# Kernel optimization log

Hardware: AMD Instinct MI355X
Metric: run time of the kernel (lower is better)

Reference implementation:

```python
import jax, jax.numpy as jnp
import numpy as np

DN = ('NCDHW', 'OIDHW', 'NCDHW')  # torch Conv3d layout

def conv3d(x, w, b, pad):
    y = jax.lax.conv_general_dilated(x, w, (1, 1, 1), [(p, p) for p in pad], dimension_numbers=DN)
    return y + b[None, :, None, None, None]

def setup_inputs() -> dict:
    key = jax.random.key(0)
    ks = jax.random.split(key, 10)
    C, Cq = 64, 8  # in_channels, in_channels // 8
    s = 0.05
    x = jax.random.normal(ks[0], (2, C, 16, 16, 16), dtype=jnp.float32)
    return {
        'x': x,
        'wq': jax.random.normal(ks[1], (Cq, C, 1, 3, 1), jnp.float32) * s,
        'bq': jax.random.normal(ks[2], (Cq,), jnp.float32) * s,
        'wk': jax.random.normal(ks[3], (Cq, C, 3, 1, 1), jnp.float32) * s,
        'bk': jax.random.normal(ks[4], (Cq,), jnp.float32) * s,
        'wj': jax.random.normal(ks[5], (Cq, C, 1, 1, 3), jnp.float32) * s,
        'bj': jax.random.normal(ks[6], (Cq,), jnp.float32) * s,
        'wv': jax.random.normal(ks[7], (C, C, 1, 1, 1), jnp.float32) * s,
        'bv': jax.random.normal(ks[8], (C,), jnp.float32) * s,
        'gamma': jax.random.normal(ks[9], (1,), jnp.float32) * s,
    }

def reference(x, wq, bq, wk, bk, wj, bj, wv, bv, gamma):
    B, C, H, W, D = x.shape
    N = H * W * D
    q = conv3d(x, wq, bq, (0, 1, 0)).reshape(B, -1, N)   # [B, c, N]
    k = conv3d(x, wk, bk, (1, 0, 0)).reshape(B, -1, N)   # [B, c, N]
    j = conv3d(x, wj, bj, (0, 0, 1)).reshape(B, -1, N)   # [B, c, N]
    # affinity = (Q^T K) (J^T K) reassociated as Q^T (K J^T) K  -- identical math,
    # O(N^2 c) instead of O(N^3) since c = C//8 << N.
    kj = jnp.einsum('bcn,bdn->bcd', k, j)                # [B, c, c] = K @ J^T
    aff = jnp.einsum('bcn,bcd,bdm->bnm', q, kj, k)       # [B, N, N]
    aff = jax.nn.softmax(aff, axis=-1)
    v = conv3d(x, wv, bv, (0, 0, 0)).reshape(B, C, N)    # [B, C, N]
    weights = jnp.einsum('bcn,bnm->bcm', v, aff).reshape(B, C, H, W, D)
    return gamma * weights + x
```

## Files before the change

kernel.cpp:

```cpp
#include <hip/hip_runtime.h>

#define N 4096
#define CIN 64
#define NB 2

typedef unsigned short u16;
typedef short bf16x8 __attribute__((ext_vector_type(8)));
typedef float f32x4 __attribute__((ext_vector_type(4)));

#define OFF_QT 0
#define OFF_KT (OFF_QT + NB*N*8)
#define OFF_JT (OFF_KT + NB*N*8)
#define OFF_V  (OFF_JT + NB*N*8)
#define OFF_QK (OFF_V + NB*CIN*N)
#define OFF_MX (OFF_QK + NB*N*8)
#define OFF_SC (OFF_MX + NB*N)

__device__ __forceinline__ u16 f2bf(float f) {
    union { float f; unsigned u; } v; v.f = f;
    unsigned r = (v.u + 0x7fffu + ((v.u >> 16) & 1u)) >> 16;
    return (u16)r;
}

__global__ __launch_bounds__(256) void prep(
        const float* __restrict__ x,
        const float* __restrict__ wq, const float* __restrict__ bq,
        const float* __restrict__ wk, const float* __restrict__ bk,
        const float* __restrict__ wj, const float* __restrict__ bj,
        const float* __restrict__ wv, const float* __restrict__ bv,
        float* __restrict__ ws, u16* __restrict__ vbf, float* __restrict__ out) {
    int n = blockIdx.x * 256 + threadIdx.x;
    int y = blockIdx.y;
    int b = blockIdx.z;
    const float* xb = x + (size_t)b * CIN * N + n;

    if (y < 8) {
        int cq = y;
        int d = n & 15, w = (n >> 4) & 15, h = n >> 8;
        int owl = (w > 0) ? -16 : 0,  owh = (w < 15) ? 16 : 0;
        int ohl = (h > 0) ? -256 : 0, ohh = (h < 15) ? 256 : 0;
        int odl = (d > 0) ? -1 : 0,   odh = (d < 15) ? 1 : 0;
        float mwl = (w > 0) ? 1.f : 0.f, mwh = (w < 15) ? 1.f : 0.f;
        float mhl = (h > 0) ? 1.f : 0.f, mhh = (h < 15) ? 1.f : 0.f;
        float mdl = (d > 0) ? 1.f : 0.f, mdh = (d < 15) ? 1.f : 0.f;
        float q = bq[cq], k = bk[cq], j = bj[cq];
        for (int c0 = 0; c0 < CIN; c0 += 8) {
            float xc[8], xwl[8], xwh[8], xhl[8], xhh[8], xdl[8], xdh[8];
#pragma unroll
            for (int u = 0; u < 8; ++u) {
                const float* p = xb + (size_t)(c0 + u) * N;
                xc[u]  = p[0];
                xwl[u] = p[owl]; xwh[u] = p[owh];
                xhl[u] = p[ohl]; xhh[u] = p[ohh];
                xdl[u] = p[odl]; xdh[u] = p[odh];
            }
#pragma unroll
            for (int u = 0; u < 8; ++u) {
                int c = c0 + u;
                const float* wqr = wq + (cq * CIN + c) * 3;
                const float* wkr = wk + (cq * CIN + c) * 3;
                const float* wjr = wj + (cq * CIN + c) * 3;
                q += wqr[0] * (xwl[u] * mwl) + wqr[1] * xc[u] + wqr[2] * (xwh[u] * mwh);
                k += wkr[0] * (xhl[u] * mhl) + wkr[1] * xc[u] + wkr[2] * (xhh[u] * mhh);
                j += wjr[0] * (xdl[u] * mdl) + wjr[1] * xc[u] + wjr[2] * (xdh[u] * mdh);
            }
        }
        size_t base = (size_t)(b * N + n) * 8 + cq;
        ws[OFF_QT + base] = q;
        ws[OFF_KT + base] = k;
        ws[OFF_JT + base] = j;
    } else {
        int yy = y - 8;
        int co0 = yy * 8;
        float acc[8];
#pragma unroll
        for (int i = 0; i < 8; ++i) acc[i] = bv[co0 + i];
        for (int c0 = 0; c0 < CIN; c0 += 8) {
            float xv[8];
#pragma unroll
            for (int u = 0; u < 8; ++u) xv[u] = xb[(size_t)(c0 + u) * N];
#pragma unroll
            for (int u = 0; u < 8; ++u)
#pragma unroll
                for (int i = 0; i < 8; ++i)
                    acc[i] += wv[(co0 + i) * CIN + c0 + u] * xv[u];
            if ((c0 >> 3) == yy) {
#pragma unroll
                for (int u = 0; u < 8; ++u)
                    out[(size_t)(b * CIN + c0 + u) * N + n] = xv[u];
            }
        }
#pragma unroll
        for (int i = 0; i < 8; ++i)
            vbf[(size_t)(b * CIN + co0 + i) * N + n] = f2bf(acc[i]);
    }
}

__global__ __launch_bounds__(256) void kjqkj(const float* __restrict__ ws_in,
                                             float* __restrict__ ws) {
    __shared__ float kjpart[4][64];
    __shared__ float kjs[64];
    const int t = threadIdx.x, lane = t & 63, wid = t >> 6;
    const int b = blockIdx.y;
    const float* ktb = ws_in + OFF_KT + (size_t)b * N * 8;
    const float* jtb = ws_in + OFF_JT + (size_t)b * N * 8;
    const float* qtb = ws_in + OFF_QT + (size_t)b * N * 8;

    float acc[64];
#pragma unroll
    for (int i = 0; i < 64; ++i) acc[i] = 0.f;
    for (int i = 0; i < 16; ++i) {
        int nn = i * 256 + t;
        const float4* kt = (const float4*)(ktb + (size_t)nn * 8);
        const float4* jt = (const float4*)(jtb + (size_t)nn * 8);
        float4 ka = kt[0], kb = kt[1], ja = jt[0], jb = jt[1];
        float kv[8] = {ka.x, ka.y, ka.z, ka.w, kb.x, kb.y, kb.z, kb.w};
        float jv[8] = {ja.x, ja.y, ja.z, ja.w, jb.x, jb.y, jb.z, jb.w};
#pragma unroll
        for (int c = 0; c < 8; ++c)
#pragma unroll
            for (int dd = 0; dd < 8; ++dd) acc[c * 8 + dd] += kv[c] * jv[dd];
    }
#pragma unroll
    for (int s = 32; s >= 1; s >>= 1)
#pragma unroll
        for (int i = 0; i < 64; ++i) acc[i] += __shfl_down(acc[i], s, 64);
    if (lane == 0) {
#pragma unroll
        for (int i = 0; i < 64; ++i) kjpart[wid][i] = acc[i];
    }
    __syncthreads();
    if (t < 64) kjs[t] = kjpart[0][t] + kjpart[1][t] + kjpart[2][t] + kjpart[3][t];
    __syncthreads();

    float kjr[64];
#pragma unroll
    for (int i = 0; i < 64; ++i) kjr[i] = kjs[i];
    int m = blockIdx.x * 256 + t;
    const float4* qt = (const float4*)(qtb + (size_t)m * 8);
    float4 qa = qt[0], qb = qt[1];
    float qv[8] = {qa.x, qa.y, qa.z, qa.w, qb.x, qb.y, qb.z, qb.w};
    float o[8];
#pragma unroll
    for (int dd = 0; dd < 8; ++dd) {
        float a = 0.f;
#pragma unroll
        for (int c = 0; c < 8; ++c) a += qv[c] * kjr[c * 8 + dd];
        o[dd] = a;
    }
    float4* dst = (float4*)(ws + OFF_QK + (size_t)(b * N + m) * 8);
    dst[0] = make_float4(o[0], o[1], o[2], o[3]);
    dst[1] = make_float4(o[4], o[5], o[6], o[7]);
}

__global__ __launch_bounds__(256) void pass1(const float* __restrict__ ws,
                                             float* __restrict__ mx_o, float* __restrict__ sc_o,
                                             const float* __restrict__ gamma) {
    int wid = threadIdx.x >> 6, lane = threadIdx.x & 63;
    int gw = blockIdx.x * 4 + wid;
    int r0 = gw * 4;
    int b = r0 >> 12;
    float4 qa[4], qb[4];
#pragma unroll
    for (int rr = 0; rr < 4; ++rr) {
        const float4* q4 = (const float4*)(ws + OFF_QK + (size_t)(r0 + rr) * 8);
        qa[rr] = q4[0]; qb[rr] = q4[1];
    }
    const float* ktb = ws + OFF_KT + (size_t)b * N * 8;
    float mx[4], sm[4];
#pragma unroll
    for (int rr = 0; rr < 4; ++rr) { mx[rr] = -3.0e38f; sm[rr] = 0.f; }
#pragma unroll 4
    for (int i = 0; i < 64; ++i) {
        int m = i * 64 + lane;
        const float4* kk4 = (const float4*)(ktb + (size_t)m * 8);
        float4 ka = kk4[0], kb = kk4[1];
#pragma unroll
        for (int rr = 0; rr < 4; ++rr) {
            float a = qa[rr].x * ka.x + qa[rr].y * ka.y + qa[rr].z * ka.z + qa[rr].w * ka.w
                    + qb[rr].x * kb.x + qb[rr].y * kb.y + qb[rr].z * kb.z + qb[rr].w * kb.w;
            float nm = fmaxf(mx[rr], a);
            sm[rr] = sm[rr] * __expf(mx[rr] - nm) + __expf(a - nm);
            mx[rr] = nm;
        }
    }
#pragma unroll
    for (int s = 32; s >= 1; s >>= 1)
#pragma unroll
        for (int rr = 0; rr < 4; ++rr) {
            float omx = __shfl_xor(mx[rr], s, 64);
            float osm = __shfl_xor(sm[rr], s, 64);
            float nm = fmaxf(mx[rr], omx);
            sm[rr] = sm[rr] * __expf(mx[rr] - nm) + osm * __expf(omx - nm);
            mx[rr] = nm;
        }
    if (lane == 0) {
        float g = gamma[0];
#pragma unroll
        for (int rr = 0; rr < 4; ++rr) {
            mx_o[r0 + rr] = mx[rr];
            sc_o[r0 + rr] = g / sm[rr];
        }
    }
}

__global__ __launch_bounds__(256) void pass2(const float* __restrict__ ws,
                                             const u16* __restrict__ vbf,
                                             float* __restrict__ out) {
    __shared__ u16 Pt[64][72];
    __shared__ u16 Vt[64][72];
    __shared__ float ks[64][8];
    const int t  = threadIdx.x;
    const int b  = blockIdx.z;
    const int m0 = blockIdx.x * 64;
    const int ns = blockIdx.y;
    const float* qkT = ws + OFF_QK + (size_t)b * N * 8;
    const float* ktb = ws + OFF_KT + (size_t)b * N * 8;
    const float* mxv = ws + OFF_MX + (size_t)b * N;
    const float* scv = ws + OFF_SC + (size_t)b * N;
    const u16*   vb  = vbf + (size_t)b * CIN * N;

    if (t < 128) ((float4*)ks)[t] = ((const float4*)(ktb + (size_t)m0 * 8))[t];

    const int lane = t & 63;
    const int wid  = t >> 6;
    const int l16  = lane & 15;
    const int lq   = lane >> 4;
    const int vc   = t >> 3;
    const int vseg = t & 7;

    f32x4 acc[4];
#pragma unroll
    for (int i = 0; i < 4; ++i) acc[i] = (f32x4){0.f, 0.f, 0.f, 0.f};

    for (int ch = 0; ch < 8; ++ch) {
        const int n0 = ns * 512 + ch * 64;
        const int n  = n0 + lane;
        const float4* q4 = (const float4*)(qkT + (size_t)n * 8);
        float4 qa = q4[0], qb = q4[1];
        float mxl = mxv[n], sl = scv[n];
        uint4 v0 = *(const uint4*)(vb + (size_t)vc        * N + n0 + vseg * 8);
        uint4 v1 = *(const uint4*)(vb + (size_t)(vc + 32) * N + n0 + vseg * 8);
        __syncthreads();
#pragma unroll
        for (int r = 0; r < 16; ++r) {
            int mi = wid * 16 + r;
            float4 k0 = *(const float4*)&ks[mi][0];
            float4 k1 = *(const float4*)&ks[mi][4];
            float a = qa.x * k0.x + qa.y * k0.y + qa.z * k0.z + qa.w * k0.w
                    + qb.x * k1.x + qb.y * k1.y + qb.z * k1.z + qb.w * k1.w;
            Pt[mi][lane] = f2bf(__expf(a - mxl) * sl);
        }
        *(uint4*)&Vt[vc][vseg * 8]      = v0;
        *(uint4*)&Vt[vc + 32][vseg * 8] = v1;
        __syncthreads();
#pragma unroll
        for (int kk = 0; kk < 2; ++kk) {
            int k0i = kk * 32 + lq * 8;
            bf16x8 bfrag = *(const bf16x8*)&Pt[wid * 16 + l16][k0i];
#pragma unroll
            for (int ct = 0; ct < 4; ++ct) {
                bf16x8 afrag = *(const bf16x8*)&Vt[ct * 16 + l16][k0i];
                acc[ct] = __builtin_amdgcn_mfma_f32_16x16x32_bf16(afrag, bfrag, acc[ct], 0, 0, 0);
            }
        }
    }
    float* ob = out + (size_t)b * CIN * N;
    const int mcol = m0 + wid * 16 + l16;
#pragma unroll
    for (int ct = 0; ct < 4; ++ct)
#pragma unroll
        for (int r = 0; r < 4; ++r) {
            int c = ct * 16 + lq * 4 + r;
            atomicAdd(&ob[(size_t)c * N + mcol], acc[ct][r]);
        }
}

extern "C" void kernel_launch(void* const* d_in, const int* in_sizes, int n_in,
                              void* d_out, int out_size, void* d_ws, size_t ws_size,
                              hipStream_t stream) {
    const float* x  = (const float*)d_in[0];
    const float* wq = (const float*)d_in[1];
    const float* bq = (const float*)d_in[2];
    const float* wk = (const float*)d_in[3];
    const float* bk = (const float*)d_in[4];
    const float* wj = (const float*)d_in[5];
    const float* bj = (const float*)d_in[6];
    const float* wv = (const float*)d_in[7];
    const float* bv = (const float*)d_in[8];
    const float* gamma = (const float*)d_in[9];
    float* ws  = (float*)d_ws;
    float* out = (float*)d_out;
    u16* vbf = (u16*)(ws + OFF_V);

    prep<<<dim3(16, 16, 2), 256, 0, stream>>>(x, wq, bq, wk, bk, wj, bj, wv, bv, ws, vbf, out);
    kjqkj<<<dim3(16, 2), 256, 0, stream>>>(ws, ws);
    pass1<<<512, 256, 0, stream>>>(ws, ws + OFF_MX, ws + OFF_SC, gamma);
    pass2<<<dim3(64, 8, 2), 256, 0, stream>>>(ws, vbf, out);
}
```

Before: 155.9 us.

## Fuse four kernels into one persistent kernel with grid barriers

Merges prep, kjqkj, pass1 and pass2 into a single 512-block kernel that uses atomic-counter grid barriers between phases, so three kernel launches and their gaps are gone. Each block now recomputes the KJ reduction redundantly and computes QK for its own rows inline before the softmax statistics. Pass2 moves from 1024 blocks over 512-column chunks to 512 blocks over 1024-column chunks, which halves the atomic adds but lowers parallelism. The design depends on all 512 blocks being resident at once (launch_bounds 256,2) and adds a memset to reset the barrier counters.

New measurement: 243.5 us. 56.2% more time.

```diff
diff --git a/kernel.cpp b/kernel.cpp
--- a/kernel.cpp
+++ b/kernel.cpp
@@ -3,6 +3,7 @@
 #define N 4096
 #define CIN 64
 #define NB 2
+#define NBLK 512u
 
 typedef unsigned short u16;
 typedef short bf16x8 __attribute__((ext_vector_type(8)));
@@ -15,6 +16,7 @@
 #define OFF_QK (OFF_V + NB*CIN*N)
 #define OFF_MX (OFF_QK + NB*N*8)
 #define OFF_SC (OFF_MX + NB*N)
+#define OFF_BAR (OFF_SC + NB*N)
 
 __device__ __forceinline__ u16 f2bf(float f) {
     union { float f; unsigned u; } v; v.f = f;
@@ -22,258 +24,275 @@
     return (u16)r;
 }
 
-__global__ __launch_bounds__(256) void prep(
+__device__ __forceinline__ void grid_barrier(unsigned* bar) {
+    __syncthreads();
+    if (threadIdx.x == 0) {
+        __hip_atomic_fetch_add(bar, 1u, __ATOMIC_RELEASE, __HIP_MEMORY_SCOPE_AGENT);
+        while (__hip_atomic_load(bar, __ATOMIC_RELAXED, __HIP_MEMORY_SCOPE_AGENT) < NBLK)
+            __builtin_amdgcn_s_sleep(2);
+        __threadfence();
+    }
+    __syncthreads();
+}
+
+struct SmemB { float kjpart[4][64]; float kjs[64]; };
+struct SmemC { u16 Pt[64][72]; u16 Vt[64][72]; float ks[64][8]; };
+union Smem { SmemB b; SmemC c; };
+
+__global__ __launch_bounds__(256, 2) void fused(
         const float* __restrict__ x,
         const float* __restrict__ wq, const float* __restrict__ bq,
         const float* __restrict__ wk, const float* __restrict__ bk,
         const float* __restrict__ wj, const float* __restrict__ bj,
         const float* __restrict__ wv, const float* __restrict__ bv,
+        const float* __restrict__ gamma,
         float* __restrict__ ws, u16* __restrict__ vbf, float* __restrict__ out) {
-    int n = blockIdx.x * 256 + threadIdx.x;
-    int y = blockIdx.y;
-    int b = blockIdx.z;
-    const float* xb = x + (size_t)b * CIN * N + n;
-
-    if (y < 8) {
-        int cq = y;
-        int d = n & 15, w = (n >> 4) & 15, h = n >> 8;
-        int owl = (w > 0) ? -16 : 0,  owh = (w < 15) ? 16 : 0;
-        int ohl = (h > 0) ? -256 : 0, ohh = (h < 15) ? 256 : 0;
-        int odl = (d > 0) ? -1 : 0,   odh = (d < 15) ? 1 : 0;
-        float mwl = (w > 0) ? 1.f : 0.f, mwh = (w < 15) ? 1.f : 0.f;
-        float mhl = (h > 0) ? 1.f : 0.f, mhh = (h < 15) ? 1.f : 0.f;
-        float mdl = (d > 0) ? 1.f : 0.f, mdh = (d < 15) ? 1.f : 0.f;
-        float q = bq[cq], k = bk[cq], j = bj[cq];
-        for (int c0 = 0; c0 < CIN; c0 += 8) {
-            float xc[8], xwl[8], xwh[8], xhl[8], xhh[8], xdl[8], xdh[8];
-#pragma unroll
-            for (int u = 0; u < 8; ++u) {
-                const float* p = xb + (size_t)(c0 + u) * N;
-                xc[u]  = p[0];
-                xwl[u] = p[owl]; xwh[u] = p[owh];
-                xhl[u] = p[ohl]; xhh[u] = p[ohh];
-                xdl[u] = p[odl]; xdh[u] = p[odh];
-            }
-#pragma unroll
-            for (int u = 0; u < 8; ++u) {
-                int c = c0 + u;
-                const float* wqr = wq + (cq * CIN + c) * 3;
-                const float* wkr = wk + (cq * CIN + c) * 3;
-                const float* wjr = wj + (cq * CIN + c) * 3;
-                q += wqr[0] * (xwl[u] * mwl) + wqr[1] * xc[u] + wqr[2] * (xwh[u] * mwh);
-                k += wkr[0] * (xhl[u] * mhl) + wkr[1] * xc[u] + wkr[2] * (xhh[u] * mhh);
-                j += wjr[0] * (xdl[u] * mdl) + wjr[1] * xc[u] + wjr[2] * (xdh[u] * mdh);
-            }
-        }
-        size_t base = (size_t)(b * N + n) * 8 + cq;
-        ws[OFF_QT + base] = q;
-        ws[OFF_KT + base] = k;
-        ws[OFF_JT + base] = j;
-    } else {
-        int yy = y - 8;
-        int co0 = yy * 8;
-        float acc[8];
-#pragma unroll
-        for (int i = 0; i < 8; ++i) acc[i] = bv[co0 + i];
-        for (int c0 = 0; c0 < CIN; c0 += 8) {
-            float xv[8];
-#pragma unroll
-            for (int u = 0; u < 8; ++u) xv[u] = xb[(size_t)(c0 + u) * N];
-#pragma unroll
-            for (int u = 0; u < 8; ++u)
-#pragma unroll
-                for (int i = 0; i < 8; ++i)
-                    acc[i] += wv[(co0 + i) * CIN + c0 + u] * xv[u];
-            if ((c0 >> 3) == yy) {
+    __shared__ __align__(16) Smem shm;
+    const int t   = threadIdx.x;
+    const int blk = blockIdx.x;
+    unsigned* bar = (unsigned*)(ws + OFF_BAR);
+
+    {
+        const int bx = blk & 15;
+        const int y  = (blk >> 4) & 15;
+        const int b  = blk >> 8;
+        const int n  = bx * 256 + t;
+        const float* xb = x + (size_t)b * CIN * N + n;
+
+        if (y < 8) {
+            int cq = y;
+            int d = n & 15, w = (n >> 4) & 15, h = n >> 8;
+            int owl = (w > 0) ? -16 : 0,  owh = (w < 15) ? 16 : 0;
+            int ohl = (h > 0) ? -256 : 0, ohh = (h < 15) ? 256 : 0;
+            int odl = (d > 0) ? -1 : 0,   odh = (d < 15) ? 1 : 0;
+            float mwl = (w > 0) ? 1.f : 0.f, mwh = (w < 15) ? 1.f : 0.f;
+            float mhl = (h > 0) ? 1.f : 0.f, mhh = (h < 15) ? 1.f : 0.f;
+            float mdl = (d > 0) ? 1.f : 0.f, mdh = (d < 15) ? 1.f : 0.f;
+            float q = bq[cq], k = bk[cq], j = bj[cq];
+            for (int c0 = 0; c0 < CIN; c0 += 8) {
+                float xc[8], xwl[8], xwh[8], xhl[8], xhh[8], xdl[8], xdh[8];
+#pragma unroll
+                for (int u = 0; u < 8; ++u) {
+                    const float* p = xb + (size_t)(c0 + u) * N;
+                    xc[u]  = p[0];
+                    xwl[u] = p[owl]; xwh[u] = p[owh];
+                    xhl[u] = p[ohl]; xhh[u] = p[ohh];
+                    xdl[u] = p[odl]; xdh[u] = p[odh];
+                }
+#pragma unroll
+                for (int u = 0; u < 8; ++u) {
+                    int c = c0 + u;
+                    const float* wqr = wq + (cq * CIN + c) * 3;
+                    const float* wkr = wk + (cq * CIN + c) * 3;
+                    const float* wjr = wj + (cq * CIN + c) * 3;
+                    q += wqr[0] * (xwl[u] * mwl) + wqr[1] * xc[u] + wqr[2] * (xwh[u] * mwh);
+                    k += wkr[0] * (xhl[u] * mhl) + wkr[1] * xc[u] + wkr[2] * (xhh[u] * mhh);
+                    j += wjr[0] * (xdl[u] * mdl) + wjr[1] * xc[u] + wjr[2] * (xdh[u] * mdh);
+                }
+            }
+            size_t base = (size_t)(b * N + n) * 8 + cq;
+            ws[OFF_QT + base] = q;
+            ws[OFF_KT + base] = k;
+            ws[OFF_JT + base] = j;
+        } else {
+            int yy = y - 8;
+            int co0 = yy * 8;
+            float acc[8];
+#pragma unroll
+            for (int i = 0; i < 8; ++i) acc[i] = bv[co0 + i];
+            for (int c0 = 0; c0 < CIN; c0 += 8) {
+                float xv[8];
+#pragma unroll
+                for (int u = 0; u < 8; ++u) xv[u] = xb[(size_t)(c0 + u) * N];
 #pragma unroll
                 for (int u = 0; u < 8; ++u)
-                    out[(size_t)(b * CIN + c0 + u) * N + n] = xv[u];
-            }
-        }
-#pragma unroll
-        for (int i = 0; i < 8; ++i)
-            vbf[(size_t)(b * CIN + co0 + i) * N + n] = f2bf(acc[i]);
+#pragma unroll
+                    for (int i = 0; i < 8; ++i)
+                        acc[i] += wv[(co0 + i) * CIN + c0 + u] * xv[u];
+                if ((c0 >> 3) == yy) {
+#pragma unroll
+                    for (int u = 0; u < 8; ++u)
+                        out[(size_t)(b * CIN + c0 + u) * N + n] = xv[u];
+                }
+            }
+#pragma unroll
+            for (int i = 0; i < 8; ++i)
+                vbf[(size_t)(b * CIN + co0 + i) * N + n] = f2bf(acc[i]);
+        }
     }
-}
-
-__global__ __launch_bounds__(256) void kjqkj(const float* __restrict__ ws_in,
-                                             float* __restrict__ ws) {
-    __shared__ float kjpart[4][64];
-    __shared__ float kjs[64];
-    const int t = threadIdx.x, lane = t & 63, wid = t >> 6;
-    const int b = blockIdx.y;
-    const float* ktb = ws_in + OFF_KT + (size_t)b * N * 8;
-    const float* jtb = ws_in + OFF_JT + (size_t)b * N * 8;
-    const float* qtb = ws_in + OFF_QT + (size_t)b * N * 8;
-
-    float acc[64];
-#pragma unroll
-    for (int i = 0; i < 64; ++i) acc[i] = 0.f;
-    for (int i = 0; i < 16; ++i) {
-        int nn = i * 256 + t;
-        const float4* kt = (const float4*)(ktb + (size_t)nn * 8);
-        const float4* jt = (const float4*)(jtb + (size_t)nn * 8);
-        float4 ka = kt[0], kb = kt[1], ja = jt[0], jb = jt[1];
-        float kv[8] = {ka.x, ka.y, ka.z, ka.w, kb.x, kb.y, kb.z, kb.w};
-        float jv[8] = {ja.x, ja.y, ja.z, ja.w, jb.x, jb.y, jb.z, jb.w};
-#pragma unroll
-        for (int c = 0; c < 8; ++c)
-#pragma unroll
-            for (int dd = 0; dd < 8; ++dd) acc[c * 8 + dd] += kv[c] * jv[dd];
+
+    grid_barrier(bar + 0);
+
+    {
+        const int lane = t & 63, wid = t >> 6;
+        const int b    = blk >> 8;
+        const float* ktb = ws + OFF_KT + (size_t)b * N * 8;
+        const float* jtb = ws + OFF_JT + (size_t)b * N * 8;
+
+        float acc[64];
+#pragma unroll
+        for (int i = 0; i < 64; ++i) acc[i] = 0.f;
+        for (int i = 0; i < 16; ++i) {
+            int nn = i * 256 + t;
+            const float4* kt = (const float4*)(ktb + (size_t)nn * 8);
+            const float4* jt = (const float4*)(jtb + (size_t)nn * 8);
+            float4 ka = kt[0], kb2 = kt[1], ja = jt[0], jb2 = jt[1];
+            float kv[8] = {ka.x, ka.y, ka.z, ka.w, kb2.x, kb2.y, kb2.z, kb2.w};
+            float jv[8] = {ja.x, ja.y, ja.z, ja.w, jb2.x, jb2.y, jb2.z, jb2.w};
+#pragma unroll
+            for (int c = 0; c < 8; ++c)
+#pragma unroll
+                for (int dd = 0; dd < 8; ++dd) acc[c * 8 + dd] += kv[c] * jv[dd];
+        }
+#pragma unroll
+        for (int s = 32; s >= 1; s >>= 1)
+#pragma unroll
+            for (int i = 0; i < 64; ++i) acc[i] += __shfl_down(acc[i], s, 64);
+        if (lane == 0) {
+#pragma unroll
+            for (int i = 0; i < 64; ++i) shm.b.kjpart[wid][i] = acc[i];
+        }
+        __syncthreads();
+        if (t < 64)
+            shm.b.kjs[t] = shm.b.kjpart[0][t] + shm.b.kjpart[1][t]
+                         + shm.b.kjpart[2][t] + shm.b.kjpart[3][t];
+        __syncthreads();
+
+        float kjr[64];
+#pragma unroll
+        for (int i = 0; i < 64; ++i) kjr[i] = shm.b.kjs[i];
+        const int r0 = blk * 16 + wid * 4;
+        float4 qa[4], qb[4];
+#pragma unroll
+        for (int rr = 0; rr < 4; ++rr) {
+            const float4* q4 = (const float4*)(ws + OFF_QT + (size_t)(r0 + rr) * 8);
+            float4 a4 = q4[0], b4 = q4[1];
+            float qv[8] = {a4.x, a4.y, a4.z, a4.w, b4.x, b4.y, b4.z, b4.w};
+            float o[8];
+#pragma unroll
+            for (int dd = 0; dd < 8; ++dd) {
+                float a = 0.f;
+#pragma unroll
+                for (int c = 0; c < 8; ++c) a += qv[c] * kjr[c * 8 + dd];
+                o[dd] = a;
+            }
+            qa[rr] = make_float4(o[0], o[1], o[2], o[3]);
+            qb[rr] = make_float4(o[4], o[5], o[6], o[7]);
+        }
+        if (lane < 32) {
+            const int rr = lane >> 3, dd = lane & 7;
+            const float* qr = ws + OFF_QT + (size_t)(r0 + rr) * 8;
+            float o = 0.f;
+#pragma unroll
+            for (int c = 0; c < 8; ++c) o += qr[c] * shm.b.kjs[c * 8 + dd];
+            ws[OFF_QK + (size_t)r0 * 8 + lane] = o;
+        }
+
+        float mx[4], sm2[4];
+#pragma unroll
+        for (int rr = 0; rr < 4; ++rr) { mx[rr] = -3.0e38f; sm2[rr] = 0.f; }
+#pragma unroll 4
+        for (int i = 0; i < 64; ++i) {
+            const int m = i * 64 + lane;
+            const float4* kk4 = (const float4*)(ktb + (size_t)m * 8);
+            float4 ka = kk4[0], kb2 = kk4[1];
+#pragma unroll
+            for (int rr = 0; rr < 4; ++rr) {
+                float a = qa[rr].x * ka.x + qa[rr].y * ka.y + qa[rr].z * ka.z + qa[rr].w * ka.w
+                        + qb[rr].x * kb2.x + qb[rr].y * kb2.y + qb[rr].z * kb2.z + qb[rr].w * kb2.w;
+                float nm = fmaxf(mx[rr], a);
+                sm2[rr] = sm2[rr] * __expf(mx[rr] - nm) + __expf(a - nm);
+                mx[rr] = nm;
+            }
+        }
+#pragma unroll
+        for (int s = 32; s >= 1; s >>= 1)
+#pragma unroll
+            for (int rr = 0; rr < 4; ++rr) {
+                float omx = __shfl_xor(mx[rr], s, 64);
+                float osm = __shfl_xor(sm2[rr], s, 64);
+                float nm = fmaxf(mx[rr], omx);
+                sm2[rr] = sm2[rr] * __expf(mx[rr] - nm) + osm * __expf(omx - nm);
+                mx[rr] = nm;
+            }
+        if (lane == 0) {
+            float g = gamma[0];
+#pragma unroll
+            for (int rr = 0; rr < 4; ++rr) {
+                ws[OFF_MX + r0 + rr] = mx[rr];
+                ws[OFF_SC + r0 + rr] = g / sm2[rr];
+            }
+        }
     }
-#pragma unroll
-    for (int s = 32; s >= 1; s >>= 1)
-#pragma unroll
-        for (int i = 0; i < 64; ++i) acc[i] += __shfl_down(acc[i], s, 64);
-    if (lane == 0) {
-#pragma unroll
-        for (int i = 0; i < 64; ++i) kjpart[wid][i] = acc[i];
+
+    grid_barrier(bar + 1);
+
+    {
+        const int mt = blk & 63;
+        const int ns = (blk >> 6) & 3;
+        const int b  = blk >> 8;
+        const int m0 = mt * 64;
+        const float* qkT = ws + OFF_QK + (size_t)b * N * 8;
+        const float* ktb = ws + OFF_KT + (size_t)b * N * 8;
+        const float* mxv = ws + OFF_MX + (size_t)b * N;
+        const float* scv = ws + OFF_SC + (size_t)b * N;
+        const u16*   vb  = vbf + (size_t)b * CIN * N;
+
+        if (t < 128) ((float4*)shm.c.ks)[t] = ((const float4*)(ktb + (size_t)m0 * 8))[t];
+
+        const int lane = t & 63;
+        const int wid  = t >> 6;
+        const int l16  = lane & 15;
+        const int lq   = lane >> 4;
+        const int vc   = t >> 3;
+        const int vseg = t & 7;
+
+        f32x4 acc[4];
+#pragma unroll
+        for (int i = 0; i < 4; ++i) acc[i] = (f32x4){0.f, 0.f, 0.f, 0.f};
+
+        for (int ch = 0; ch < 16; ++ch) {
+            const int n0 = ns * 1024 + ch * 64;
+            const int n  = n0 + lane;
+            const float4* q4 = (const float4*)(qkT + (size_t)n * 8);
+            float4 qa = q4[0], qb = q4[1];
+            float mxl = mxv[n], sl = scv[n];
+            uint4 v0 = *(const uint4*)(vb + (size_t)vc        * N + n0 + vseg * 8);
+            uint4 v1 = *(const uint4*)(vb + (size_t)(vc + 32) * N + n0 + vseg * 8);
+            __syncthreads();
+#pragma unroll
+            for (int r = 0; r < 16; ++r) {
+                int mi = wid * 16 + r;
+                float4 k0 = *(const float4*)&shm.c.ks[mi][0];
+                float4 k1 = *(const float4*)&shm.c.ks[mi][4];
+                float a = qa.x * k0.x + qa.y * k0.y + qa.z * k0.z + qa.w * k0.w
+                        + qb.x * k1.x + qb.y * k1.y + qb.z * k1.z + qb.w * k1.w;
+                shm.c.Pt[mi][lane] = f2bf(__expf(a - mxl) * sl);
+            }
+            *(uint4*)&shm.c.Vt[vc][vseg * 8]      = v0;
+            *(uint4*)&shm.c.Vt[vc + 32][vseg * 8] = v1;
+            __syncthreads();
+#pragma unroll
+            for (int kk = 0; kk < 2; ++kk) {
+                int k0i = kk * 32 + lq * 8;
+                bf16x8 bfrag = *(const bf16x8*)&shm.c.Pt[wid * 16 + l16][k0i];
+#pragma unroll
+                for (int ct = 0; ct < 4; ++ct) {
+                    bf16x8 afrag = *(const bf16x8*)&shm.c.Vt[ct * 16 + l16][k0i];
+                    acc[ct] = __builtin_amdgcn_mfma_f32_16x16x32_bf16(afrag, bfrag, acc[ct], 0, 0, 0);
+                }
+            }
+        }
+        float* ob = out + (size_t)b * CIN * N;
+        const int mcol = m0 + wid * 16 + l16;
+#pragma unroll
+        for (int ct = 0; ct < 4; ++ct)
+#pragma unroll
+            for (int r = 0; r < 4; ++r) {
+                int c = ct * 16 + lq * 4 + r;
+                atomicAdd(&ob[(size_t)c * N + mcol], acc[ct][r]);
+            }
     }
-    __syncthreads();
-    if (t < 64) kjs[t] = kjpart[0][t] + kjpart[1][t] + kjpart[2][t] + kjpart[3][t];
-    __syncthreads();
-
-    float kjr[64];
-#pragma unroll
-    for (int i = 0; i < 64; ++i) kjr[i] = kjs[i];
-    int m = blockIdx.x * 256 + t;
-    const float4* qt = (const float4*)(qtb + (size_t)m * 8);
-    float4 qa = qt[0], qb = qt[1];
-    float qv[8] = {qa.x, qa.y, qa.z, qa.w, qb.x, qb.y, qb.z, qb.w};
-    float o[8];
-#pragma unroll
-    for (int dd = 0; dd < 8; ++dd) {
-        float a = 0.f;
-#pragma unroll
-        for (int c = 0; c < 8; ++c) a += qv[c] * kjr[c * 8 + dd];
-        o[dd] = a;
-    }
-    float4* dst = (float4*)(ws + OFF_QK + (size_t)(b * N + m) * 8);
-    dst[0] = make_float4(o[0], o[1], o[2], o[3]);
-    dst[1] = make_float4(o[4], o[5], o[6], o[7]);
-}
-
-__global__ __launch_bounds__(256) void pass1(const float* __restrict__ ws,
-                                             float* __restrict__ mx_o, float* __restrict__ sc_o,
-                                             const float* __restrict__ gamma) {
-    int wid = threadIdx.x >> 6, lane = threadIdx.x & 63;
-    int gw = blockIdx.x * 4 + wid;
-    int r0 = gw * 4;
-    int b = r0 >> 12;
-    float4 qa[4], qb[4];
-#pragma unroll
-    for (int rr = 0; rr < 4; ++rr) {
-        const float4* q4 = (const float4*)(ws + OFF_QK + (size_t)(r0 + rr) * 8);
-        qa[rr] = q4[0]; qb[rr] = q4[1];
-    }
-    const float* ktb = ws + OFF_KT + (size_t)b * N * 8;
-    float mx[4], sm[4];
-#pragma unroll
-    for (int rr = 0; rr < 4; ++rr) { mx[rr] = -3.0e38f; sm[rr] = 0.f; }
-#pragma unroll 4
-    for (int i = 0; i < 64; ++i) {
-        int m = i * 64 + lane;
-        const float4* kk4 = (const float4*)(ktb + (size_t)m * 8);
-        float4 ka = kk4[0], kb = kk4[1];
-#pragma unroll
-        for (int rr = 0; rr < 4; ++rr) {
-            float a = qa[rr].x * ka.x + qa[rr].y * ka.y + qa[rr].z * ka.z + qa[rr].w * ka.w
-                    + qb[rr].x * kb.x + qb[rr].y * kb.y + qb[rr].z * kb.z + qb[rr].w * kb.w;
-            float nm = fmaxf(mx[rr], a);
-            sm[rr] = sm[rr] * __expf(mx[rr] - nm) + __expf(a - nm);
-            mx[rr] = nm;
-        }
-    }
-#pragma unroll
-    for (int s = 32; s >= 1; s >>= 1)
-#pragma unroll
-        for (int rr = 0; rr < 4; ++rr) {
-            float omx = __shfl_xor(mx[rr], s, 64);
-            float osm = __shfl_xor(sm[rr], s, 64);
-            float nm = fmaxf(mx[rr], omx);
-            sm[rr] = sm[rr] * __expf(mx[rr] - nm) + osm * __expf(omx - nm);
-            mx[rr] = nm;
-        }
-    if (lane == 0) {
-        float g = gamma[0];
-#pragma unroll
-        for (int rr = 0; rr < 4; ++rr) {
-            mx_o[r0 + rr] = mx[rr];
-            sc_o[r0 + rr] = g / sm[rr];
-        }
-    }
-}
-
-__global__ __launch_bounds__(256) void pass2(const float* __restrict__ ws,
-                                             const u16* __restrict__ vbf,
-                                             float* __restrict__ out) {
-    __shared__ u16 Pt[64][72];
-    __shared__ u16 Vt[64][72];
-    __shared__ float ks[64][8];
-    const int t  = threadIdx.x;
-    const int b  = blockIdx.z;
-    const int m0 = blockIdx.x * 64;
-    const int ns = blockIdx.y;
-    const float* qkT = ws + OFF_QK + (size_t)b * N * 8;
-    const float* ktb = ws + OFF_KT + (size_t)b * N * 8;
-    const float* mxv = ws + OFF_MX + (size_t)b * N;
-    const float* scv = ws + OFF_SC + (size_t)b * N;
-    const u16*   vb  = vbf + (size_t)b * CIN * N;
-
-    if (t < 128) ((float4*)ks)[t] = ((const float4*)(ktb + (size_t)m0 * 8))[t];
-
-    const int lane = t & 63;
-    const int wid  = t >> 6;
-    const int l16  = lane & 15;
-    const int lq   = lane >> 4;
-    const int vc   = t >> 3;
-    const int vseg = t & 7;
-
-    f32x4 acc[4];
-#pragma unroll
-    for (int i = 0; i < 4; ++i) acc[i] = (f32x4){0.f, 0.f, 0.f, 0.f};
-
-    for (int ch = 0; ch < 8; ++ch) {
-        const int n0 = ns * 512 + ch * 64;
-        const int n  = n0 + lane;
-        const float4* q4 = (const float4*)(qkT + (size_t)n * 8);
-        float4 qa = q4[0], qb = q4[1];
-        float mxl = mxv[n], sl = scv[n];
-        uint4 v0 = *(const uint4*)(vb + (size_t)vc        * N + n0 + vseg * 8);
-        uint4 v1 = *(const uint4*)(vb + (size_t)(vc + 32) * N + n0 + vseg * 8);
-        __syncthreads();
-#pragma unroll
-        for (int r = 0; r < 16; ++r) {
-            int mi = wid * 16 + r;
-            float4 k0 = *(const float4*)&ks[mi][0];
-            float4 k1 = *(const float4*)&ks[mi][4];
-            float a = qa.x * k0.x + qa.y * k0.y + qa.z * k0.z + qa.w * k0.w
-                    + qb.x * k1.x + qb.y * k1.y + qb.z * k1.z + qb.w * k1.w;
-            Pt[mi][lane] = f2bf(__expf(a - mxl) * sl);
-        }
-        *(uint4*)&Vt[vc][vseg * 8]      = v0;
-        *(uint4*)&Vt[vc + 32][vseg * 8] = v1;
-        __syncthreads();
-#pragma unroll
-        for (int kk = 0; kk < 2; ++kk) {
-            int k0i = kk * 32 + lq * 8;
-            bf16x8 bfrag = *(const bf16x8*)&Pt[wid * 16 + l16][k0i];
-#pragma unroll
-            for (int ct = 0; ct < 4; ++ct) {
-                bf16x8 afrag = *(const bf16x8*)&Vt[ct * 16 + l16][k0i];
-                acc[ct] = __builtin_amdgcn_mfma_f32_16x16x32_bf16(afrag, bfrag, acc[ct], 0, 0, 0);
-            }
-        }
-    }
-    float* ob = out + (size_t)b * CIN * N;
-    const int mcol = m0 + wid * 16 + l16;
-#pragma unroll
-    for (int ct = 0; ct < 4; ++ct)
-#pragma unroll
-        for (int r = 0; r < 4; ++r) {
-            int c = ct * 16 + lq * 4 + r;
-            atomicAdd(&ob[(size_t)c * N + mcol], acc[ct][r]);
-        }
 }
 
 extern "C" void kernel_launch(void* const* d_in, const int* in_sizes, int n_in,
@@ -293,8 +312,7 @@
     float* out = (float*)d_out;
     u16* vbf = (u16*)(ws + OFF_V);
 
-    prep<<<dim3(16, 16, 2), 256, 0, stream>>>(x, wq, bq, wk, bk, wj, bj, wv, bv, ws, vbf, out);
-    kjqkj<<<dim3(16, 2), 256, 0, stream>>>(ws, ws);
-    pass1<<<512, 256, 0, stream>>>(ws, ws + OFF_MX, ws + OFF_SC, gamma);
-    pass2<<<dim3(64, 8, 2), 256, 0, stream>>>(ws, vbf, out);
+    hipMemsetAsync(ws + OFF_BAR, 0, 2 * sizeof(unsigned), stream);
+    fused<<<dim3(512), dim3(256), 0, stream>>>(x, wq, bq, wk, bk, wj, bj, wv, bv,
+                                               gamma, ws, vbf, out);
 }
```

## Fuse KJ/QK computation into softmax stats kernel and split channel reduction in prep

Applied to the files above, without the earlier changes.

Merges the kjqkj and pass1 kernels into one statsB kernel. Each block recomputes the 8x8 K·J^T product redundantly, derives its own QK rows, and splits the key range across two half-blocks whose partial max/sum are merged in shared memory. The prep kernel also moves to 512 threads, with each half summing 32 input channels and the halves combined through shared memory. The goal is to drop one launch and improve parallelism, at the cost of recomputing the KJ reduction over all N in each of the 512 blocks.

After: 178.2 us. +14.3%, slower.

```diff
diff --git a/kernel.cpp b/kernel.cpp
--- a/kernel.cpp
+++ b/kernel.cpp
@@ -22,17 +22,25 @@
     return (u16)r;
 }
 
-__global__ __launch_bounds__(256) void prep(
+__global__ __launch_bounds__(512, 4) void prep(
         const float* __restrict__ x,
         const float* __restrict__ wq, const float* __restrict__ bq,
         const float* __restrict__ wk, const float* __restrict__ bk,
         const float* __restrict__ wj, const float* __restrict__ bj,
         const float* __restrict__ wv, const float* __restrict__ bv,
         float* __restrict__ ws, u16* __restrict__ vbf, float* __restrict__ out) {
-    int n = blockIdx.x * 256 + threadIdx.x;
-    int y = blockIdx.y;
-    int b = blockIdx.z;
+    __shared__ union {
+        float qkj[3][256];
+        float accv[256][8];
+    } sh;
+    const int t    = threadIdx.x;
+    const int tn   = t & 255;
+    const int half = t >> 8;
+    const int y    = blockIdx.y;
+    const int b    = blockIdx.z;
+    const int n    = blockIdx.x * 256 + tn;
     const float* xb = x + (size_t)b * CIN * N + n;
+    const int c0base = half * 32;
 
     if (y < 8) {
         int cq = y;
@@ -43,8 +51,11 @@
         float mwl = (w > 0) ? 1.f : 0.f, mwh = (w < 15) ? 1.f : 0.f;
         float mhl = (h > 0) ? 1.f : 0.f, mhh = (h < 15) ? 1.f : 0.f;
         float mdl = (d > 0) ? 1.f : 0.f, mdh = (d < 15) ? 1.f : 0.f;
-        float q = bq[cq], k = bk[cq], j = bj[cq];
-        for (int c0 = 0; c0 < CIN; c0 += 8) {
+        float q = half ? 0.f : bq[cq];
+        float k = half ? 0.f : bk[cq];
+        float j = half ? 0.f : bj[cq];
+        for (int c0i = 0; c0i < 32; c0i += 8) {
+            const int c0 = c0base + c0i;
             float xc[8], xwl[8], xwh[8], xhl[8], xhh[8], xdl[8], xdh[8];
 #pragma unroll
             for (int u = 0; u < 8; ++u) {
@@ -65,17 +76,23 @@
                 j += wjr[0] * (xdl[u] * mdl) + wjr[1] * xc[u] + wjr[2] * (xdh[u] * mdh);
             }
         }
-        size_t base = (size_t)(b * N + n) * 8 + cq;
-        ws[OFF_QT + base] = q;
-        ws[OFF_KT + base] = k;
-        ws[OFF_JT + base] = j;
+        if (half) { sh.qkj[0][tn] = q; sh.qkj[1][tn] = k; sh.qkj[2][tn] = j; }
+        __syncthreads();
+        if (!half) {
+            q += sh.qkj[0][tn]; k += sh.qkj[1][tn]; j += sh.qkj[2][tn];
+            size_t base = (size_t)(b * N + n) * 8 + cq;
+            ws[OFF_QT + base] = q;
+            ws[OFF_KT + base] = k;
+            ws[OFF_JT + base] = j;
+        }
     } else {
         int yy = y - 8;
         int co0 = yy * 8;
         float acc[8];
 #pragma unroll
-        for (int i = 0; i < 8; ++i) acc[i] = bv[co0 + i];
-        for (int c0 = 0; c0 < CIN; c0 += 8) {
+        for (int i = 0; i < 8; ++i) acc[i] = half ? 0.f : bv[co0 + i];
+        for (int c0i = 0; c0i < 32; c0i += 8) {
+            const int c0 = c0base + c0i;
             float xv[8];
 #pragma unroll
             for (int u = 0; u < 8; ++u) xv[u] = xb[(size_t)(c0 + u) * N];
@@ -90,32 +107,40 @@
                     out[(size_t)(b * CIN + c0 + u) * N + n] = xv[u];
             }
         }
-#pragma unroll
-        for (int i = 0; i < 8; ++i)
-            vbf[(size_t)(b * CIN + co0 + i) * N + n] = f2bf(acc[i]);
-    }
-}
-
-__global__ __launch_bounds__(256) void kjqkj(const float* __restrict__ ws_in,
-                                             float* __restrict__ ws) {
-    __shared__ float kjpart[4][64];
+        if (half) {
+#pragma unroll
+            for (int i = 0; i < 8; ++i) sh.accv[tn][i] = acc[i];
+        }
+        __syncthreads();
+        if (!half) {
+#pragma unroll
+            for (int i = 0; i < 8; ++i)
+                vbf[(size_t)(b * CIN + co0 + i) * N + n] = f2bf(acc[i] + sh.accv[tn][i]);
+        }
+    }
+}
+
+__global__ __launch_bounds__(512, 4) void statsB(float* __restrict__ ws,
+                                                 const float* __restrict__ gamma) {
+    __shared__ float kjpart[8][64];
     __shared__ float kjs[64];
+    __shared__ float mxs[8][4], sms[8][4];
     const int t = threadIdx.x, lane = t & 63, wid = t >> 6;
-    const int b = blockIdx.y;
-    const float* ktb = ws_in + OFF_KT + (size_t)b * N * 8;
-    const float* jtb = ws_in + OFF_JT + (size_t)b * N * 8;
-    const float* qtb = ws_in + OFF_QT + (size_t)b * N * 8;
+    const int blk = blockIdx.x;
+    const int b   = blk >> 8;
+    const float* ktb = ws + OFF_KT + (size_t)b * N * 8;
+    const float* jtb = ws + OFF_JT + (size_t)b * N * 8;
 
     float acc[64];
 #pragma unroll
     for (int i = 0; i < 64; ++i) acc[i] = 0.f;
-    for (int i = 0; i < 16; ++i) {
-        int nn = i * 256 + t;
+    for (int i = 0; i < 8; ++i) {
+        int nn = i * 512 + t;
         const float4* kt = (const float4*)(ktb + (size_t)nn * 8);
         const float4* jt = (const float4*)(jtb + (size_t)nn * 8);
-        float4 ka = kt[0], kb = kt[1], ja = jt[0], jb = jt[1];
-        float kv[8] = {ka.x, ka.y, ka.z, ka.w, kb.x, kb.y, kb.z, kb.w};
-        float jv[8] = {ja.x, ja.y, ja.z, ja.w, jb.x, jb.y, jb.z, jb.w};
+        float4 ka = kt[0], kb2 = kt[1], ja = jt[0], jb2 = jt[1];
+        float kv[8] = {ka.x, ka.y, ka.z, ka.w, kb2.x, kb2.y, kb2.z, kb2.w};
+        float jv[8] = {ja.x, ja.y, ja.z, ja.w, jb2.x, jb2.y, jb2.z, jb2.w};
 #pragma unroll
         for (int c = 0; c < 8; ++c)
 #pragma unroll
@@ -130,57 +155,57 @@
         for (int i = 0; i < 64; ++i) kjpart[wid][i] = acc[i];
     }
     __syncthreads();
-    if (t < 64) kjs[t] = kjpart[0][t] + kjpart[1][t] + kjpart[2][t] + kjpart[3][t];
+    if (t < 64)
+        kjs[t] = kjpart[0][t] + kjpart[1][t] + kjpart[2][t] + kjpart[3][t]
+               + kjpart[4][t] + kjpart[5][t] + kjpart[6][t] + kjpart[7][t];
     __syncthreads();
 
     float kjr[64];
 #pragma unroll
     for (int i = 0; i < 64; ++i) kjr[i] = kjs[i];
-    int m = blockIdx.x * 256 + t;
-    const float4* qt = (const float4*)(qtb + (size_t)m * 8);
-    float4 qa = qt[0], qb = qt[1];
-    float qv[8] = {qa.x, qa.y, qa.z, qa.w, qb.x, qb.y, qb.z, qb.w};
-    float o[8];
-#pragma unroll
-    for (int dd = 0; dd < 8; ++dd) {
-        float a = 0.f;
-#pragma unroll
-        for (int c = 0; c < 8; ++c) a += qv[c] * kjr[c * 8 + dd];
-        o[dd] = a;
-    }
-    float4* dst = (float4*)(ws + OFF_QK + (size_t)(b * N + m) * 8);
-    dst[0] = make_float4(o[0], o[1], o[2], o[3]);
-    dst[1] = make_float4(o[4], o[5], o[6], o[7]);
-}
-
-__global__ __launch_bounds__(256) void pass1(const float* __restrict__ ws,
-                                             float* __restrict__ mx_o, float* __restrict__ sc_o,
-                                             const float* __restrict__ gamma) {
-    int wid = threadIdx.x >> 6, lane = threadIdx.x & 63;
-    int gw = blockIdx.x * 4 + wid;
-    int r0 = gw * 4;
-    int b = r0 >> 12;
+    const int wrow  = wid & 3;
+    const int mhalf = wid >> 2;
+    const int r0 = blk * 16 + wrow * 4;
     float4 qa[4], qb[4];
 #pragma unroll
     for (int rr = 0; rr < 4; ++rr) {
-        const float4* q4 = (const float4*)(ws + OFF_QK + (size_t)(r0 + rr) * 8);
-        qa[rr] = q4[0]; qb[rr] = q4[1];
-    }
-    const float* ktb = ws + OFF_KT + (size_t)b * N * 8;
-    float mx[4], sm[4];
-#pragma unroll
-    for (int rr = 0; rr < 4; ++rr) { mx[rr] = -3.0e38f; sm[rr] = 0.f; }
+        const float4* q4 = (const float4*)(ws + OFF_QT + (size_t)(r0 + rr) * 8);
+        float4 a4 = q4[0], b4 = q4[1];
+        float qv[8] = {a4.x, a4.y, a4.z, a4.w, b4.x, b4.y, b4.z, b4.w};
+        float o[8];
+#pragma unroll
+        for (int dd = 0; dd < 8; ++dd) {
+            float a = 0.f;
+#pragma unroll
+            for (int c = 0; c < 8; ++c) a += qv[c] * kjr[c * 8 + dd];
+            o[dd] = a;
+        }
+        qa[rr] = make_float4(o[0], o[1], o[2], o[3]);
+        qb[rr] = make_float4(o[4], o[5], o[6], o[7]);
+    }
+    if (mhalf == 0 && lane < 32) {
+        const int rr = lane >> 3, dd = lane & 7;
+        const float* qr = ws + OFF_QT + (size_t)(r0 + rr) * 8;
+        float o = 0.f;
+#pragma unroll
+        for (int c = 0; c < 8; ++c) o += qr[c] * kjs[c * 8 + dd];
+        ws[OFF_QK + (size_t)r0 * 8 + lane] = o;
+    }
+
+    float mx[4], sm2[4];
+#pragma unroll
+    for (int rr = 0; rr < 4; ++rr) { mx[rr] = -3.0e38f; sm2[rr] = 0.f; }
 #pragma unroll 4
-    for (int i = 0; i < 64; ++i) {
-        int m = i * 64 + lane;
+    for (int i = 0; i < 32; ++i) {
+        const int m = mhalf * 2048 + i * 64 + lane;
         const float4* kk4 = (const float4*)(ktb + (size_t)m * 8);
-        float4 ka = kk4[0], kb = kk4[1];
+        float4 ka = kk4[0], kb2 = kk4[1];
 #pragma unroll
         for (int rr = 0; rr < 4; ++rr) {
             float a = qa[rr].x * ka.x + qa[rr].y * ka.y + qa[rr].z * ka.z + qa[rr].w * ka.w
-                    + qb[rr].x * kb.x + qb[rr].y * kb.y + qb[rr].z * kb.z + qb[rr].w * kb.w;
+                    + qb[rr].x * kb2.x + qb[rr].y * kb2.y + qb[rr].z * kb2.z + qb[rr].w * kb2.w;
             float nm = fmaxf(mx[rr], a);
-            sm[rr] = sm[rr] * __expf(mx[rr] - nm) + __expf(a - nm);
+            sm2[rr] = sm2[rr] * __expf(mx[rr] - nm) + __expf(a - nm);
             mx[rr] = nm;
         }
     }
@@ -189,18 +214,24 @@
 #pragma unroll
         for (int rr = 0; rr < 4; ++rr) {
             float omx = __shfl_xor(mx[rr], s, 64);
-            float osm = __shfl_xor(sm[rr], s, 64);
+            float osm = __shfl_xor(sm2[rr], s, 64);
             float nm = fmaxf(mx[rr], omx);
-            sm[rr] = sm[rr] * __expf(mx[rr] - nm) + osm * __expf(omx - nm);
+            sm2[rr] = sm2[rr] * __expf(mx[rr] - nm) + osm * __expf(omx - nm);
             mx[rr] = nm;
         }
     if (lane == 0) {
-        float g = gamma[0];
-#pragma unroll
-        for (int rr = 0; rr < 4; ++rr) {
-            mx_o[r0 + rr] = mx[rr];
-            sc_o[r0 + rr] = g / sm[rr];
-        }
+#pragma unroll
+        for (int rr = 0; rr < 4; ++rr) { mxs[wid][rr] = mx[rr]; sms[wid][rr] = sm2[rr]; }
+    }
+    __syncthreads();
+    if (t < 16) {
+        const int w = t >> 2, rr = t & 3;
+        float m1 = mxs[w][rr], m2 = mxs[w + 4][rr];
+        float s1 = sms[w][rr], s2 = sms[w + 4][rr];
+        float nm = fmaxf(m1, m2);
+        float sm = s1 * __expf(m1 - nm) + s2 * __expf(m2 - nm);
+        ws[OFF_MX + blk * 16 + w * 4 + rr] = nm;
+        ws[OFF_SC + blk * 16 + w * 4 + rr] = gamma[0] / sm;
     }
 }
 
@@ -293,8 +324,7 @@
     float* out = (float*)d_out;
     u16* vbf = (u16*)(ws + OFF_V);
 
-    prep<<<dim3(16, 16, 2), 256, 0, stream>>>(x, wq, bq, wk, bk, wj, bj, wv, bv, ws, vbf, out);
-    kjqkj<<<dim3(16, 2), 256, 0, stream>>>(ws, ws);
-    pass1<<<512, 256, 0, stream>>>(ws, ws + OFF_MX, ws + OFF_SC, gamma);
+    prep<<<dim3(16, 16, 2), 512, 0, stream>>>(x, wq, bq, wk, bk, wj, bj, wv, bv, ws, vbf, out);
+    statsB<<<512, 512, 0, stream>>>(ws, gamma);
     pass2<<<dim3(64, 8, 2), 256, 0, stream>>>(ws, vbf, out);
 }
```

## Split prep channel reduction and pass1 key range across more waves

Applied to the files above, without the earlier changes.

The prep kernel now runs 512 threads per block. Each half reduces 32 of the 64 input channels, and the two partial sums are combined through shared memory. Pass1 now splits each row's 4096 keys across four waves and uses a two-pass softmax: it finds the max with a cross-wave reduction, then sums the exponentials. The aim is more parallelism and shorter serial chains in two low-occupancy, latency-bound kernels, at the cost of block-level syncs, extra shared memory, and 64 live score registers per thread in pass1.

Measured after the change: 212.3 us. 36.2% more time.

```diff
diff --git a/kernel.cpp b/kernel.cpp
--- a/kernel.cpp
+++ b/kernel.cpp
@@ -22,17 +22,25 @@
     return (u16)r;
 }
 
-__global__ __launch_bounds__(256) void prep(
+__global__ __launch_bounds__(512, 4) void prep(
         const float* __restrict__ x,
         const float* __restrict__ wq, const float* __restrict__ bq,
         const float* __restrict__ wk, const float* __restrict__ bk,
         const float* __restrict__ wj, const float* __restrict__ bj,
         const float* __restrict__ wv, const float* __restrict__ bv,
         float* __restrict__ ws, u16* __restrict__ vbf, float* __restrict__ out) {
-    int n = blockIdx.x * 256 + threadIdx.x;
-    int y = blockIdx.y;
-    int b = blockIdx.z;
+    __shared__ union {
+        float qkj[3][256];
+        float accv[256][8];
+    } sh;
+    const int t    = threadIdx.x;
+    const int tn   = t & 255;
+    const int half = t >> 8;
+    const int y    = blockIdx.y;
+    const int b    = blockIdx.z;
+    const int n    = blockIdx.x * 256 + tn;
     const float* xb = x + (size_t)b * CIN * N + n;
+    const int c0base = half * 32;
 
     if (y < 8) {
         int cq = y;
@@ -43,8 +51,11 @@
         float mwl = (w > 0) ? 1.f : 0.f, mwh = (w < 15) ? 1.f : 0.f;
         float mhl = (h > 0) ? 1.f : 0.f, mhh = (h < 15) ? 1.f : 0.f;
         float mdl = (d > 0) ? 1.f : 0.f, mdh = (d < 15) ? 1.f : 0.f;
-        float q = bq[cq], k = bk[cq], j = bj[cq];
-        for (int c0 = 0; c0 < CIN; c0 += 8) {
+        float q = half ? 0.f : bq[cq];
+        float k = half ? 0.f : bk[cq];
+        float j = half ? 0.f : bj[cq];
+        for (int c0i = 0; c0i < 32; c0i += 8) {
+            const int c0 = c0base + c0i;
             float xc[8], xwl[8], xwh[8], xhl[8], xhh[8], xdl[8], xdh[8];
 #pragma unroll
             for (int u = 0; u < 8; ++u) {
@@ -65,17 +76,23 @@
                 j += wjr[0] * (xdl[u] * mdl) + wjr[1] * xc[u] + wjr[2] * (xdh[u] * mdh);
             }
         }
-        size_t base = (size_t)(b * N + n) * 8 + cq;
-        ws[OFF_QT + base] = q;
-        ws[OFF_KT + base] = k;
-        ws[OFF_JT + base] = j;
+        if (half) { sh.qkj[0][tn] = q; sh.qkj[1][tn] = k; sh.qkj[2][tn] = j; }
+        __syncthreads();
+        if (!half) {
+            q += sh.qkj[0][tn]; k += sh.qkj[1][tn]; j += sh.qkj[2][tn];
+            size_t base = (size_t)(b * N + n) * 8 + cq;
+            ws[OFF_QT + base] = q;
+            ws[OFF_KT + base] = k;
+            ws[OFF_JT + base] = j;
+        }
     } else {
         int yy = y - 8;
         int co0 = yy * 8;
         float acc[8];
 #pragma unroll
-        for (int i = 0; i < 8; ++i) acc[i] = bv[co0 + i];
-        for (int c0 = 0; c0 < CIN; c0 += 8) {
+        for (int i = 0; i < 8; ++i) acc[i] = half ? 0.f : bv[co0 + i];
+        for (int c0i = 0; c0i < 32; c0i += 8) {
+            const int c0 = c0base + c0i;
             float xv[8];
 #pragma unroll
             for (int u = 0; u < 8; ++u) xv[u] = xb[(size_t)(c0 + u) * N];
@@ -90,9 +107,16 @@
                     out[(size_t)(b * CIN + c0 + u) * N + n] = xv[u];
             }
         }
-#pragma unroll
-        for (int i = 0; i < 8; ++i)
-            vbf[(size_t)(b * CIN + co0 + i) * N + n] = f2bf(acc[i]);
+        if (half) {
+#pragma unroll
+            for (int i = 0; i < 8; ++i) sh.accv[tn][i] = acc[i];
+        }
+        __syncthreads();
+        if (!half) {
+#pragma unroll
+            for (int i = 0; i < 8; ++i)
+                vbf[(size_t)(b * CIN + co0 + i) * N + n] = f2bf(acc[i] + sh.accv[tn][i]);
+        }
     }
 }
 
@@ -153,54 +177,92 @@
     dst[1] = make_float4(o[4], o[5], o[6], o[7]);
 }
 
-__global__ __launch_bounds__(256) void pass1(const float* __restrict__ ws,
-                                             float* __restrict__ mx_o, float* __restrict__ sc_o,
-                                             const float* __restrict__ gamma) {
-    int wid = threadIdx.x >> 6, lane = threadIdx.x & 63;
-    int gw = blockIdx.x * 4 + wid;
-    int r0 = gw * 4;
-    int b = r0 >> 12;
+__global__ __launch_bounds__(512, 4) void pass1(const float* __restrict__ ws,
+                                                float* __restrict__ mx_o, float* __restrict__ sc_o,
+                                                const float* __restrict__ gamma) {
+    __shared__ float smx[4][8];
+    __shared__ float ssum[4][8];
+    const int t = threadIdx.x, lane = t & 63, wid = t >> 6;
+    const int rowgrp = wid & 1;
+    const int mq     = wid >> 1;
+    const int R0 = blockIdx.x * 8;
+    const int b  = R0 >> 12;
+    const int r0 = R0 + rowgrp * 4;
+    const float* ktb = ws + OFF_KT + (size_t)b * N * 8;
+
     float4 qa[4], qb[4];
 #pragma unroll
     for (int rr = 0; rr < 4; ++rr) {
         const float4* q4 = (const float4*)(ws + OFF_QK + (size_t)(r0 + rr) * 8);
         qa[rr] = q4[0]; qb[rr] = q4[1];
     }
-    const float* ktb = ws + OFF_KT + (size_t)b * N * 8;
-    float mx[4], sm[4];
-#pragma unroll
-    for (int rr = 0; rr < 4; ++rr) { mx[rr] = -3.0e38f; sm[rr] = 0.f; }
+
+    float as[4][16];
 #pragma unroll 4
-    for (int i = 0; i < 64; ++i) {
-        int m = i * 64 + lane;
+    for (int i = 0; i < 16; ++i) {
+        const int m = mq * 1024 + i * 64 + lane;
         const float4* kk4 = (const float4*)(ktb + (size_t)m * 8);
-        float4 ka = kk4[0], kb = kk4[1];
-#pragma unroll
-        for (int rr = 0; rr < 4; ++rr) {
-            float a = qa[rr].x * ka.x + qa[rr].y * ka.y + qa[rr].z * ka.z + qa[rr].w * ka.w
-                    + qb[rr].x * kb.x + qb[rr].y * kb.y + qb[rr].z * kb.z + qb[rr].w * kb.w;
-            float nm = fmaxf(mx[rr], a);
-            sm[rr] = sm[rr] * __expf(mx[rr] - nm) + __expf(a - nm);
-            mx[rr] = nm;
-        }
+        float4 ka = kk4[0], kb2 = kk4[1];
+#pragma unroll
+        for (int rr = 0; rr < 4; ++rr)
+            as[rr][i] = qa[rr].x * ka.x + qa[rr].y * ka.y + qa[rr].z * ka.z + qa[rr].w * ka.w
+                      + qb[rr].x * kb2.x + qb[rr].y * kb2.y + qb[rr].z * kb2.z + qb[rr].w * kb2.w;
+    }
+
+    float mx[4];
+#pragma unroll
+    for (int rr = 0; rr < 4; ++rr) {
+        float m01 = fmaxf(fmaxf(as[rr][0], as[rr][1]), fmaxf(as[rr][2], as[rr][3]));
+        float m23 = fmaxf(fmaxf(as[rr][4], as[rr][5]), fmaxf(as[rr][6], as[rr][7]));
+        float m45 = fmaxf(fmaxf(as[rr][8], as[rr][9]), fmaxf(as[rr][10], as[rr][11]));
+        float m67 = fmaxf(fmaxf(as[rr][12], as[rr][13]), fmaxf(as[rr][14], as[rr][15]));
+        mx[rr] = fmaxf(fmaxf(m01, m23), fmaxf(m45, m67));
     }
 #pragma unroll
     for (int s = 32; s >= 1; s >>= 1)
 #pragma unroll
-        for (int rr = 0; rr < 4; ++rr) {
-            float omx = __shfl_xor(mx[rr], s, 64);
-            float osm = __shfl_xor(sm[rr], s, 64);
-            float nm = fmaxf(mx[rr], omx);
-            sm[rr] = sm[rr] * __expf(mx[rr] - nm) + osm * __expf(omx - nm);
-            mx[rr] = nm;
-        }
+        for (int rr = 0; rr < 4; ++rr)
+            mx[rr] = fmaxf(mx[rr], __shfl_xor(mx[rr], s, 64));
     if (lane == 0) {
-        float g = gamma[0];
-#pragma unroll
-        for (int rr = 0; rr < 4; ++rr) {
-            mx_o[r0 + rr] = mx[rr];
-            sc_o[r0 + rr] = g / sm[rr];
-        }
+#pragma unroll
+        for (int rr = 0; rr < 4; ++rr) smx[mq][rowgrp * 4 + rr] = mx[rr];
+    }
+    __syncthreads();
+    float gm[4];
+#pragma unroll
+    for (int rr = 0; rr < 4; ++rr) {
+        const int ri = rowgrp * 4 + rr;
+        gm[rr] = fmaxf(fmaxf(smx[0][ri], smx[1][ri]), fmaxf(smx[2][ri], smx[3][ri]));
+    }
+
+    float sm[4];
+#pragma unroll
+    for (int rr = 0; rr < 4; ++rr) {
+        float s0 = __expf(as[rr][0] - gm[rr])  + __expf(as[rr][1] - gm[rr])
+                 + __expf(as[rr][2] - gm[rr])  + __expf(as[rr][3] - gm[rr]);
+        float s1 = __expf(as[rr][4] - gm[rr])  + __expf(as[rr][5] - gm[rr])
+                 + __expf(as[rr][6] - gm[rr])  + __expf(as[rr][7] - gm[rr]);
+        float s2 = __expf(as[rr][8] - gm[rr])  + __expf(as[rr][9] - gm[rr])
+                 + __expf(as[rr][10] - gm[rr]) + __expf(as[rr][11] - gm[rr]);
+        float s3 = __expf(as[rr][12] - gm[rr]) + __expf(as[rr][13] - gm[rr])
+                 + __expf(as[rr][14] - gm[rr]) + __expf(as[rr][15] - gm[rr]);
+        sm[rr] = (s0 + s1) + (s2 + s3);
+    }
+#pragma unroll
+    for (int s = 32; s >= 1; s >>= 1)
+#pragma unroll
+        for (int rr = 0; rr < 4; ++rr)
+            sm[rr] += __shfl_xor(sm[rr], s, 64);
+    if (lane == 0) {
+#pragma unroll
+        for (int rr = 0; rr < 4; ++rr) ssum[mq][rowgrp * 4 + rr] = sm[rr];
+    }
+    __syncthreads();
+    if (t < 8) {
+        float g  = fmaxf(fmaxf(smx[0][t], smx[1][t]), fmaxf(smx[2][t], smx[3][t]));
+        float tt = (ssum[0][t] + ssum[1][t]) + (ssum[2][t] + ssum[3][t]);
+        mx_o[R0 + t] = g;
+        sc_o[R0 + t] = gamma[0] / tt;
     }
 }
 
@@ -293,8 +355,8 @@
     float* out = (float*)d_out;
     u16* vbf = (u16*)(ws + OFF_V);
 
-    prep<<<dim3(16, 16, 2), 256, 0, stream>>>(x, wq, bq, wk, bk, wj, bj, wv, bv, ws, vbf, out);
+    prep<<<dim3(16, 16, 2), 512, 0, stream>>>(x, wq, bq, wk, bk, wj, bj, wv, bv, ws, vbf, out);
     kjqkj<<<dim3(16, 2), 256, 0, stream>>>(ws, ws);
-    pass1<<<512, 256, 0, stream>>>(ws, ws + OFF_MX, ws + OFF_SC, gamma);
+    pass1<<<1024, 512, 0, stream>>>(ws, ws + OFF_MX, ws + OFF_SC, gamma);
     pass2<<<dim3(64, 8, 2), 256, 0, stream>>>(ws, vbf, out);
 }
```
